# Kernel optimization log

Measured on AMD Instinct MI355X. Metric: run time of the kernel, lower is better.

Reference implementation:

```python
import jax, jax.numpy as jnp
import numpy as np

BOS_IDX = 1


def setup_inputs() -> dict:
    key = jax.random.key(0)
    ks = jax.random.split(key, 12)
    B, T, S, H, L, V = 16, 128, 64, 512, 2, 32000
    s = 0.05
    return {
        "encoder_outputs": jax.random.normal(ks[0], (B, S, H), jnp.float32),
        "encoder_h": jax.random.normal(ks[1], (L, B, H), jnp.float32) * s,
        "encoder_c": jax.random.normal(ks[2], (L, B, H), jnp.float32) * s,
        "target_tensor": jax.random.randint(ks[3], (B, T), 0, V),
        "embedding": jax.random.normal(ks[4], (V, H), jnp.float32) * s,
        "W_ih": jax.random.normal(ks[5], (L, 4 * H, H), jnp.float32) * s,
        "W_hh": jax.random.normal(ks[6], (L, 4 * H, H), jnp.float32) * s,
        "b_ih": jax.random.normal(ks[7], (L, 4 * H), jnp.float32) * s,
        "b_hh": jax.random.normal(ks[8], (L, 4 * H), jnp.float32) * s,
        "W_out": jax.random.normal(ks[9], (V, H), jnp.float32) * s,
        "b_out": jax.random.normal(ks[10], (V,), jnp.float32) * s,
    }


def reference(encoder_outputs, encoder_h, encoder_c, target_tensor,
              embedding, W_ih, W_hh, b_ih, b_hh, W_out, b_out):
    B, T = target_tensor.shape
    L = W_ih.shape[0]
    # Teacher-forced inputs: BOS then target[:, :-1]
    tokens = jnp.concatenate(
        [jnp.full((B, 1), BOS_IDX, dtype=target_tensor.dtype),
         target_tensor[:, :-1]], axis=1)  # [B, T]
    x = jax.nn.relu(embedding[tokens])  # [B, T, H]
    # The original loop resets (h, c) to encoder_states at EVERY step, so all
    # T single-step LSTM cells are independent -> vectorize over T.
    h_last, c_last = [], []
    for l in range(L):
        h0 = encoder_h[l]  # [B, H]
        c0 = encoder_c[l][:, None, :]  # [B, 1, H]
        gates = (jnp.einsum('bth,gh->btg', x, W_ih[l]) + b_ih[l]
                 + (jnp.einsum('bh,gh->bg', h0, W_hh[l]) + b_hh[l])[:, None, :])
        i, f, g, o = jnp.split(gates, 4, axis=-1)  # torch gate order i,f,g,o
        c = jax.nn.sigmoid(f) * c0 + jax.nn.sigmoid(i) * jnp.tanh(g)
        h = jax.nn.sigmoid(o) * jnp.tanh(c)  # [B, T, H]
        h_last.append(h[:, -1, :])
        c_last.append(c[:, -1, :])
        x = h  # input to next layer (dropout=0 / eval)
    logits = jnp.einsum('bth,vh->btv', x, W_out) + b_out  # [B, T, V]
    return logits, (jnp.stack(h_last), jnp.stack(c_last))
```

## Files before the change

kernel.cpp:

```cpp
#include <hip/hip_runtime.h>
#include <hip/hip_bf16.h>

typedef __bf16 bf16_t;
typedef __bf16 bf16x8 __attribute__((ext_vector_type(8)));
typedef __bf16 bf16x4 __attribute__((ext_vector_type(4)));
typedef float f32x4 __attribute__((ext_vector_type(4)));

#define B_ 16
#define T_ 128
#define H_ 512
#define L_ 2
#define V_ 32000
#define G_ 2048
#define M_ 2048

#define BN 128
#define BK 64

__device__ __forceinline__ float sigf(float x) { return 1.f / (1.f + __expf(-x)); }
__device__ __forceinline__ float tanhf_(float x) { return 2.f / (1.f + __expf(-2.f * x)) - 1.f; }


__global__ __launch_bounds__(256) void prep(const float* __restrict__ emb,
                                            const int* __restrict__ target,
                                            const float* __restrict__ enc_h,
                                            const float* __restrict__ W_ih,
                                            const float* __restrict__ W_hh,
                                            const float* __restrict__ b_ih,
                                            const float* __restrict__ b_hh,
                                            const float* __restrict__ W_out,
                                            bf16_t* __restrict__ x,
                                            bf16_t* __restrict__ wih_b,
                                            bf16_t* __restrict__ wout_b,
                                            float* __restrict__ biasall) {
    const int blk = blockIdx.x;
    const int tid = threadIdx.x;
    if (blk < 256) {
        int idx = blk * 256 + tid;
        int b = idx & 15;
        int c = (idx >> 4) & (G_ - 1);
        int l = idx >> 15;
        int gate = (c >> 4) & 3;
        int h = ((c >> 6) << 4) | (c & 15);
        int r = gate * H_ + h;
        const float* hrow = enc_h + ((size_t)l * B_ + b) * H_;
        const float* wrow = W_hh + ((size_t)l * G_ + r) * H_;
        float acc = b_ih[l * G_ + r] + b_hh[l * G_ + r];
        #pragma unroll 4
        for (int k = 0; k < H_; k += 4) {
            float4 hv = *(const float4*)(hrow + k);
            float4 wv = *(const float4*)(wrow + k);
            acc += hv.x * wv.x + hv.y * wv.y + hv.z * wv.z + hv.w * wv.w;
        }
        biasall[((size_t)l * B_ + b) * G_ + c] = acc;
    } else if (blk < 2304) {
        int idx = (blk - 256) * 256 + tid;
        int k4 = idx & 127;
        int c  = (idx >> 7) & (G_ - 1);
        int l  = idx >> 18;
        int gate = (c >> 4) & 3;
        int h = ((c >> 6) << 4) | (c & 15);
        int r = gate * H_ + h;
        float4 v = *(const float4*)(W_ih + ((size_t)l * G_ + r) * H_ + k4 * 4);
        bf16x4 o;
        o[0] = (bf16_t)v.x; o[1] = (bf16_t)v.y; o[2] = (bf16_t)v.z; o[3] = (bf16_t)v.w;
        *(bf16x4*)(wih_b + ((size_t)l * G_ + c) * H_ + k4 * 4) = o;
    } else if (blk < 3328) {
        int idx = (blk - 2304) * 256 + tid;
        int m  = idx >> 7;
        int h4 = (idx & 127) << 2;
        int b = m >> 7, t = m & 127;
        int tok = (t == 0) ? 1 : target[b * T_ + t - 1];
        float4 v = *(const float4*)(emb + (size_t)tok * H_ + h4);
        bf16x4 o;
        o[0] = (bf16_t)fmaxf(v.x, 0.f);
        o[1] = (bf16_t)fmaxf(v.y, 0.f);
        o[2] = (bf16_t)fmaxf(v.z, 0.f);
        o[3] = (bf16_t)fmaxf(v.w, 0.f);
        *(bf16x4*)(x + (size_t)m * H_ + h4) = o;
    } else {
        int idx = (blk - 3328) * 256 + tid;
        const float4* p = (const float4*)W_out + (size_t)idx * 2;
        float4 v0 = p[0], v1 = p[1];
        bf16x8 o;
        o[0] = (bf16_t)v0.x; o[1] = (bf16_t)v0.y; o[2] = (bf16_t)v0.z; o[3] = (bf16_t)v0.w;
        o[4] = (bf16_t)v1.x; o[5] = (bf16_t)v1.y; o[6] = (bf16_t)v1.z; o[7] = (bf16_t)v1.w;
        ((bf16x8*)wout_b)[idx] = o;
    }
}

template<int BMt>
__global__ __launch_bounds__(256) void gemm_gates(const bf16_t* __restrict__ A,
                                                  const bf16_t* __restrict__ B,
                                                  const float* __restrict__ bias,
                                                  int M, int N, int K,
                                                  const float* __restrict__ enc_c,
                                                  bf16_t* __restrict__ xout,
                                                  float* __restrict__ out_h,
                                                  float* __restrict__ out_c,
                                                  int l) {
    constexpr int MIc = BMt / 32;
    constexpr int NA  = BMt / 8;
    constexpr int NB  = BN / 8;
    __shared__ __align__(16) bf16_t As[BMt * BK];
    __shared__ __align__(16) bf16_t Bs[BN * BK];

    const int tid  = threadIdx.x;
    const int lane = tid & 63;
    const int wave = tid >> 6;
    const int wm = wave >> 1, wn = wave & 1;
    const int quad = lane >> 4;
    const int r16  = lane & 15;

    const int nwg = gridDim.x;
    const int q  = nwg >> 3;
    const int wg = (blockIdx.x & 7) * q + (blockIdx.x >> 3);
    const int nbx = M / BMt;
    const int bx = wg % nbx;
    const int by = wg / nbx;
    const int tileM = bx * BMt;
    const int tileN = by * BN;

    const int srow = lane >> 3;
    const int scol = (((lane & 7) ^ (lane >> 3)) << 3);

    f32x4 acc[MIc][4];
    #pragma unroll
    for (int i = 0; i < MIc; i++)
        #pragma unroll
        for (int j = 0; j < 4; j++) acc[i][j] = (f32x4){0.f, 0.f, 0.f, 0.f};

    const int nk = K / BK;
    for (int kt = 0; kt < nk; ++kt) {
        const int k0 = kt * BK;
        #pragma unroll
        for (int ii = 0; ii < (NA + NB) / 4; ++ii) {
            const int i = ii * 4 + wave;
            const bf16_t* src;
            bf16_t* dst;
            if (i < NA) {
                const int r0 = i * 8;
                src = A + (size_t)(tileM + r0 + srow) * K + k0 + scol;
                dst = As + r0 * BK;
            } else {
                const int r0 = (i - NA) * 8;
                src = B + (size_t)(tileN + r0 + srow) * K + k0 + scol;
                dst = Bs + r0 * BK;
            }
            __builtin_amdgcn_global_load_lds(
                (const __attribute__((address_space(1))) void*)src,
                (__attribute__((address_space(3))) void*)dst, 16, 0, 0);
        }
        __syncthreads();

        #pragma unroll
        for (int ks = 0; ks < 2; ++ks) {
            bf16x8 af[MIc], bfr[4];
            const int ub = ks * 4 + quad;
            #pragma unroll
            for (int mi = 0; mi < MIc; mi++) {
                const int row = wm * (BMt / 2) + mi * 16 + r16;
                af[mi] = *(const bf16x8*)(As + row * BK + ((ub ^ (r16 & 7)) << 3));
            }
            #pragma unroll
            for (int ni = 0; ni < 4; ni++) {
                const int row = wn * 64 + ni * 16 + r16;
                bfr[ni] = *(const bf16x8*)(Bs + row * BK + ((ub ^ (r16 & 7)) << 3));
            }
            #pragma unroll
            for (int mi = 0; mi < MIc; mi++)
                #pragma unroll
                for (int ni = 0; ni < 4; ni++)
                    acc[mi][ni] = __builtin_amdgcn_mfma_f32_16x16x32_bf16(
                        af[mi], bfr[ni], acc[mi][ni], 0, 0, 0);
        }
        __syncthreads();
    }

    const int b = tileM >> 7;
    const float* brow = bias + (size_t)b * G_;
    float bv[4];
    #pragma unroll
    for (int g = 0; g < 4; g++)
        bv[g] = brow[tileN + wn * 64 + g * 16 + r16];
    const int h = (2 * by + wn) * 16 + r16;
    const float c0 = enc_c[((size_t)l * B_ + b) * H_ + h];
    #pragma unroll
    for (int mi = 0; mi < MIc; mi++) {
        #pragma unroll
        for (int rr = 0; rr < 4; rr++) {
            const int t = (tileM & 127) + wm * (BMt / 2) + mi * 16 + quad * 4 + rr;
            const float gi = acc[mi][0][rr] + bv[0];
            const float gf = acc[mi][1][rr] + bv[1];
            const float gg = acc[mi][2][rr] + bv[2];
            const float go = acc[mi][3][rr] + bv[3];
            const float c = sigf(gf) * c0 + sigf(gi) * tanhf_(gg);
            const float hv = sigf(go) * tanhf_(c);
            xout[(size_t)(b * T_ + t) * H_ + h] = (bf16_t)hv;
            if (t == T_ - 1) {
                out_h[((size_t)l * B_ + b) * H_ + h] = hv;
                out_c[((size_t)l * B_ + b) * H_ + h] = c;
            }
        }
    }
}

#define LBM 128
#define LBN 256
#define LBK 64
#define LNK 8
__global__ __launch_bounds__(512, 1) void gemm_logits(const bf16_t* __restrict__ A,
                                                      const bf16_t* __restrict__ B,
                                                      float* __restrict__ C,
                                                      const float* __restrict__ bias) {
    __shared__ __align__(16) bf16_t Abuf[3][LBM * LBK];
    __shared__ __align__(16) bf16_t Bbuf[3][LBN * LBK];

    const int tid  = threadIdx.x;
    const int lane = tid & 63;
    const int wave = tid >> 6;
    const int wm = wave >> 2, wn = wave & 3;
    const int quad = lane >> 4;
    const int r16  = lane & 15;

    const int wg = (blockIdx.x & 7) * 250 + (blockIdx.x >> 3);
    const int tileM = (wg & 15) * LBM;
    const int tileN = (wg >> 4) * LBN;

    const int srow = lane >> 3;
    const int scol = (((lane & 7) ^ srow) << 3);

    f32x4 acc[4][4];
    #pragma unroll
    for (int i = 0; i < 4; i++)
        #pragma unroll
        for (int j = 0; j < 4; j++) acc[i][j] = (f32x4){0.f, 0.f, 0.f, 0.f};

    auto issue = [&](int t, int buf) {
        const int k0 = t * LBK;
        #pragma unroll
        for (int i = 0; i < 6; ++i) {
            const int rbase = (i < 2 ? i * 64 : (i - 2) * 64) + wave * 8;
            if (i < 2) {
                const bf16_t* src = A + (size_t)(tileM + rbase + srow) * H_ + k0 + scol;
                __builtin_amdgcn_global_load_lds(
                    (const __attribute__((address_space(1))) void*)src,
                    (__attribute__((address_space(3))) void*)(&Abuf[buf][rbase * LBK]),
                    16, 0, 0);
            } else {
                const bf16_t* src = B + (size_t)(tileN + rbase + srow) * H_ + k0 + scol;
                __builtin_amdgcn_global_load_lds(
                    (const __attribute__((address_space(1))) void*)src,
                    (__attribute__((address_space(3))) void*)(&Bbuf[buf][rbase * LBK]),
                    16, 0, 0);
            }
        }
    };

    issue(0, 0);
    issue(1, 1);
    asm volatile("s_waitcnt vmcnt(6)" ::: "memory");
    __builtin_amdgcn_sched_barrier(0);
    __builtin_amdgcn_s_barrier();
    __builtin_amdgcn_sched_barrier(0);

    #pragma unroll
    for (int j = 0; j < LNK; ++j) {
        const int jb = j % 3;
        if (j + 2 < LNK) issue(j + 2, (j + 2) % 3);
        __builtin_amdgcn_sched_barrier(0);

        bf16x8 af[4][2], bfv[4][2];
        #pragma unroll
        for (int ks = 0; ks < 2; ++ks) {
            const int ub = ks * 4 + quad;
            const int pu = (ub ^ (r16 & 7)) << 3;
            #pragma unroll
            for (int mi = 0; mi < 4; mi++)
                af[mi][ks] = *(const bf16x8*)(&Abuf[jb][(wm * 64 + mi * 16 + r16) * LBK + pu]);
            #pragma unroll
            for (int ni = 0; ni < 4; ni++)
                bfv[ni][ks] = *(const bf16x8*)(&Bbuf[jb][(wn * 64 + ni * 16 + r16) * LBK + pu]);
        }

        __builtin_amdgcn_s_setprio(1);
        #pragma unroll
        for (int ks = 0; ks < 2; ++ks)
            #pragma unroll
            for (int mi = 0; mi < 4; mi++)
                #pragma unroll
                for (int ni = 0; ni < 4; ni++)
                    acc[mi][ni] = __builtin_amdgcn_mfma_f32_16x16x32_bf16(
                        af[mi][ks], bfv[ni][ks], acc[mi][ni], 0, 0, 0);
        __builtin_amdgcn_s_setprio(0);

        if (j < LNK - 1) {
            if (j < LNK - 2) { asm volatile("s_waitcnt vmcnt(6)" ::: "memory"); }
            else             { asm volatile("s_waitcnt vmcnt(0)" ::: "memory"); }
            __builtin_amdgcn_sched_barrier(0);
            __builtin_amdgcn_s_barrier();
            __builtin_amdgcn_sched_barrier(0);
        }
    }

    #pragma unroll
    for (int mi = 0; mi < 4; mi++) {
        #pragma unroll
        for (int ni = 0; ni < 4; ni++) {
            const int col = tileN + wn * 64 + ni * 16 + r16;
            const float bv = bias[col];
            #pragma unroll
            for (int rr = 0; rr < 4; rr++) {
                const int row = tileM + wm * 64 + mi * 16 + quad * 4 + rr;
                __builtin_nontemporal_store(acc[mi][ni][rr] + bv,
                                            &C[(size_t)row * V_ + col]);
            }
        }
    }
}

extern "C" void kernel_launch(void* const* d_in, const int* in_sizes, int n_in,
                              void* d_out, int out_size, void* d_ws, size_t ws_size,
                              hipStream_t stream) {
    const float* enc_h  = (const float*)d_in[1];
    const float* enc_c  = (const float*)d_in[2];
    const int*   target = (const int*)d_in[3];
    const float* emb    = (const float*)d_in[4];
    const float* W_ih   = (const float*)d_in[5];
    const float* W_hh   = (const float*)d_in[6];
    const float* b_ih   = (const float*)d_in[7];
    const float* b_hh   = (const float*)d_in[8];
    const float* W_out  = (const float*)d_in[9];
    const float* b_out  = (const float*)d_in[10];
    float* out = (float*)d_out;

    char* w = (char*)d_ws;
    bf16_t* x       = (bf16_t*)(w);
    bf16_t* wih_b   = (bf16_t*)(w + 2097152);
    bf16_t* wout_b  = (bf16_t*)(w + 6291456);
    bf16_t* x2      = (bf16_t*)(w + 39059456);
    float*  biasall = (float*)(w + 55836672);

    float* out_h = out + (size_t)M_ * V_;
    float* out_c = out_h + (size_t)L_ * B_ * H_;

    prep<<<11328, 256, 0, stream>>>(emb, target, enc_h, W_ih, W_hh, b_ih, b_hh,
                                    W_out, x, wih_b, wout_b, biasall);

    gemm_gates<64><<<(M_ / 64) * (G_ / BN), 256, 0, stream>>>(
        x, wih_b, biasall, M_, G_, H_,
        enc_c, x2, out_h, out_c, 0);
    gemm_gates<64><<<(M_ / 64) * (G_ / BN), 256, 0, stream>>>(
        x2, wih_b + (size_t)G_ * H_, biasall + (size_t)B_ * G_,
        M_, G_, H_, enc_c, x, out_h, out_c, 1);

    gemm_logits<<<(M_ / LBM) * (V_ / LBN), 512, 0, stream>>>(x, wout_b, out, b_out);
}
```

Before: 468.5 us.

## Fuse W_out conversion into gates kernels and simplify logits GEMM to 256 threads

Moves the W_out fp32-to-bf16 conversion out of the prep kernel and splits it across the two gates kernels as extra blocks, so the memory-bound conversion can overlap with the small gate GEMMs. The gates GEMM is de-templated with hardcoded sizes. The logits GEMM drops its triple-buffered 512-thread pipeline with explicit waitcnt for a simple single-buffer 256-thread kernel with 128x256 tiles per block and more accumulators per wave. This risks losing load/compute overlap and raising register pressure in the dominant logits GEMM.

After: 504.6 us. 1.08x slower.

```diff
diff --git a/kernel.cpp b/kernel.cpp
--- a/kernel.cpp
+++ b/kernel.cpp
@@ -14,9 +14,6 @@
 #define G_ 2048
 #define M_ 2048
 
-#define BN 128
-#define BK 64
-
 __device__ __forceinline__ float sigf(float x) { return 1.f / (1.f + __expf(-x)); }
 __device__ __forceinline__ float tanhf_(float x) { return 2.f / (1.f + __expf(-2.f * x)) - 1.f; }
 
@@ -28,10 +25,8 @@
                                             const float* __restrict__ W_hh,
                                             const float* __restrict__ b_ih,
                                             const float* __restrict__ b_hh,
-                                            const float* __restrict__ W_out,
                                             bf16_t* __restrict__ x,
                                             bf16_t* __restrict__ wih_b,
-                                            bf16_t* __restrict__ wout_b,
                                             float* __restrict__ biasall) {
     const int blk = blockIdx.x;
     const int tid = threadIdx.x;
@@ -65,7 +60,7 @@
         bf16x4 o;
         o[0] = (bf16_t)v.x; o[1] = (bf16_t)v.y; o[2] = (bf16_t)v.z; o[3] = (bf16_t)v.w;
         *(bf16x4*)(wih_b + ((size_t)l * G_ + c) * H_ + k4 * 4) = o;
-    } else if (blk < 3328) {
+    } else {
         int idx = (blk - 2304) * 256 + tid;
         int m  = idx >> 7;
         int h4 = (idx & 127) << 2;
@@ -78,32 +73,32 @@
         o[2] = (bf16_t)fmaxf(v.z, 0.f);
         o[3] = (bf16_t)fmaxf(v.w, 0.f);
         *(bf16x4*)(x + (size_t)m * H_ + h4) = o;
-    } else {
-        int idx = (blk - 3328) * 256 + tid;
+    }
+}
+
+__global__ __launch_bounds__(256) void gates_cvt(const bf16_t* __restrict__ A,
+                                                 const bf16_t* __restrict__ B,
+                                                 const float* __restrict__ bias,
+                                                 const float* __restrict__ enc_c,
+                                                 bf16_t* __restrict__ xout,
+                                                 float* __restrict__ out_h,
+                                                 float* __restrict__ out_c,
+                                                 int l,
+                                                 const float* __restrict__ W_out,
+                                                 bf16_t* __restrict__ wout_b) {
+    if (blockIdx.x >= 512) {
+        int idx = (blockIdx.x - 512) * 256 + threadIdx.x + l * 1024000;
         const float4* p = (const float4*)W_out + (size_t)idx * 2;
         float4 v0 = p[0], v1 = p[1];
         bf16x8 o;
         o[0] = (bf16_t)v0.x; o[1] = (bf16_t)v0.y; o[2] = (bf16_t)v0.z; o[3] = (bf16_t)v0.w;
         o[4] = (bf16_t)v1.x; o[5] = (bf16_t)v1.y; o[6] = (bf16_t)v1.z; o[7] = (bf16_t)v1.w;
         ((bf16x8*)wout_b)[idx] = o;
-    }
-}
-
-template<int BMt>
-__global__ __launch_bounds__(256) void gemm_gates(const bf16_t* __restrict__ A,
-                                                  const bf16_t* __restrict__ B,
-                                                  const float* __restrict__ bias,
-                                                  int M, int N, int K,
-                                                  const float* __restrict__ enc_c,
-                                                  bf16_t* __restrict__ xout,
-                                                  float* __restrict__ out_h,
-                                                  float* __restrict__ out_c,
-                                                  int l) {
-    constexpr int MIc = BMt / 32;
-    constexpr int NA  = BMt / 8;
-    constexpr int NB  = BN / 8;
-    __shared__ __align__(16) bf16_t As[BMt * BK];
-    __shared__ __align__(16) bf16_t Bs[BN * BK];
+        return;
+    }
+    constexpr int BM = 64, GBN = 128, BK = 64;
+    __shared__ __align__(16) bf16_t As[BM * BK];
+    __shared__ __align__(16) bf16_t Bs[GBN * BK];
 
     const int tid  = threadIdx.x;
     const int lane = tid & 63;
@@ -112,40 +107,35 @@
     const int quad = lane >> 4;
     const int r16  = lane & 15;
 
-    const int nwg = gridDim.x;
-    const int q  = nwg >> 3;
-    const int wg = (blockIdx.x & 7) * q + (blockIdx.x >> 3);
-    const int nbx = M / BMt;
-    const int bx = wg % nbx;
-    const int by = wg / nbx;
-    const int tileM = bx * BMt;
-    const int tileN = by * BN;
+    const int wg = (blockIdx.x & 7) * 64 + (blockIdx.x >> 3);
+    const int bx = wg & 31;
+    const int by = wg >> 5;
+    const int tileM = bx * BM;
+    const int tileN = by * GBN;
 
     const int srow = lane >> 3;
-    const int scol = (((lane & 7) ^ (lane >> 3)) << 3);
-
-    f32x4 acc[MIc][4];
-    #pragma unroll
-    for (int i = 0; i < MIc; i++)
+    const int scol = (((lane & 7) ^ srow) << 3);
+
+    f32x4 acc[2][4];
+    #pragma unroll
+    for (int i = 0; i < 2; i++)
         #pragma unroll
         for (int j = 0; j < 4; j++) acc[i][j] = (f32x4){0.f, 0.f, 0.f, 0.f};
 
-    const int nk = K / BK;
-    for (int kt = 0; kt < nk; ++kt) {
+    for (int kt = 0; kt < H_ / BK; ++kt) {
         const int k0 = kt * BK;
         #pragma unroll
-        for (int ii = 0; ii < (NA + NB) / 4; ++ii) {
+        for (int ii = 0; ii < 6; ++ii) {
             const int i = ii * 4 + wave;
             const bf16_t* src;
             bf16_t* dst;
-            if (i < NA) {
-                const int r0 = i * 8;
-                src = A + (size_t)(tileM + r0 + srow) * K + k0 + scol;
-                dst = As + r0 * BK;
+            if (i < 8) {
+                src = A + (size_t)(tileM + i * 8 + srow) * H_ + k0 + scol;
+                dst = As + i * 8 * BK;
             } else {
-                const int r0 = (i - NA) * 8;
-                src = B + (size_t)(tileN + r0 + srow) * K + k0 + scol;
-                dst = Bs + r0 * BK;
+                const int j = i - 8;
+                src = B + (size_t)(tileN + j * 8 + srow) * H_ + k0 + scol;
+                dst = Bs + j * 8 * BK;
             }
             __builtin_amdgcn_global_load_lds(
                 (const __attribute__((address_space(1))) void*)src,
@@ -155,20 +145,17 @@
 
         #pragma unroll
         for (int ks = 0; ks < 2; ++ks) {
-            bf16x8 af[MIc], bfr[4];
+            bf16x8 af[2], bfr[4];
             const int ub = ks * 4 + quad;
-            #pragma unroll
-            for (int mi = 0; mi < MIc; mi++) {
-                const int row = wm * (BMt / 2) + mi * 16 + r16;
-                af[mi] = *(const bf16x8*)(As + row * BK + ((ub ^ (r16 & 7)) << 3));
-            }
-            #pragma unroll
-            for (int ni = 0; ni < 4; ni++) {
-                const int row = wn * 64 + ni * 16 + r16;
-                bfr[ni] = *(const bf16x8*)(Bs + row * BK + ((ub ^ (r16 & 7)) << 3));
-            }
-            #pragma unroll
-            for (int mi = 0; mi < MIc; mi++)
+            const int pu = (ub ^ (r16 & 7)) << 3;
+            #pragma unroll
+            for (int mi = 0; mi < 2; mi++)
+                af[mi] = *(const bf16x8*)(As + (wm * 32 + mi * 16 + r16) * BK + pu);
+            #pragma unroll
+            for (int ni = 0; ni < 4; ni++)
+                bfr[ni] = *(const bf16x8*)(Bs + (wn * 64 + ni * 16 + r16) * BK + pu);
+            #pragma unroll
+            for (int mi = 0; mi < 2; mi++)
                 #pragma unroll
                 for (int ni = 0; ni < 4; ni++)
                     acc[mi][ni] = __builtin_amdgcn_mfma_f32_16x16x32_bf16(
@@ -186,10 +173,10 @@
     const int h = (2 * by + wn) * 16 + r16;
     const float c0 = enc_c[((size_t)l * B_ + b) * H_ + h];
     #pragma unroll
-    for (int mi = 0; mi < MIc; mi++) {
+    for (int mi = 0; mi < 2; mi++) {
         #pragma unroll
         for (int rr = 0; rr < 4; rr++) {
-            const int t = (tileM & 127) + wm * (BMt / 2) + mi * 16 + quad * 4 + rr;
+            const int t = (tileM & 127) + wm * 32 + mi * 16 + quad * 4 + rr;
             const float gi = acc[mi][0][rr] + bv[0];
             const float gf = acc[mi][1][rr] + bv[1];
             const float gg = acc[mi][2][rr] + bv[2];
@@ -208,18 +195,17 @@
 #define LBM 128
 #define LBN 256
 #define LBK 64
-#define LNK 8
-__global__ __launch_bounds__(512, 1) void gemm_logits(const bf16_t* __restrict__ A,
-                                                      const bf16_t* __restrict__ B,
-                                                      float* __restrict__ C,
-                                                      const float* __restrict__ bias) {
-    __shared__ __align__(16) bf16_t Abuf[3][LBM * LBK];
-    __shared__ __align__(16) bf16_t Bbuf[3][LBN * LBK];
+__global__ __launch_bounds__(256) void gemm_logits(const bf16_t* __restrict__ A,
+                                                   const bf16_t* __restrict__ B,
+                                                   float* __restrict__ C,
+                                                   const float* __restrict__ bias) {
+    __shared__ __align__(16) bf16_t As[LBM * LBK];
+    __shared__ __align__(16) bf16_t Bs[LBN * LBK];
 
     const int tid  = threadIdx.x;
     const int lane = tid & 63;
     const int wave = tid >> 6;
-    const int wm = wave >> 2, wn = wave & 3;
+    const int wm = wave >> 1, wn = wave & 1;
     const int quad = lane >> 4;
     const int r16  = lane & 15;
 
@@ -230,84 +216,61 @@
     const int srow = lane >> 3;
     const int scol = (((lane & 7) ^ srow) << 3);
 
-    f32x4 acc[4][4];
+    f32x4 acc[4][8];
     #pragma unroll
     for (int i = 0; i < 4; i++)
         #pragma unroll
-        for (int j = 0; j < 4; j++) acc[i][j] = (f32x4){0.f, 0.f, 0.f, 0.f};
-
-    auto issue = [&](int t, int buf) {
-        const int k0 = t * LBK;
-        #pragma unroll
-        for (int i = 0; i < 6; ++i) {
-            const int rbase = (i < 2 ? i * 64 : (i - 2) * 64) + wave * 8;
-            if (i < 2) {
-                const bf16_t* src = A + (size_t)(tileM + rbase + srow) * H_ + k0 + scol;
-                __builtin_amdgcn_global_load_lds(
-                    (const __attribute__((address_space(1))) void*)src,
-                    (__attribute__((address_space(3))) void*)(&Abuf[buf][rbase * LBK]),
-                    16, 0, 0);
+        for (int j = 0; j < 8; j++) acc[i][j] = (f32x4){0.f, 0.f, 0.f, 0.f};
+
+    for (int kt = 0; kt < H_ / LBK; ++kt) {
+        const int k0 = kt * LBK;
+        #pragma unroll
+        for (int ii = 0; ii < 12; ++ii) {
+            const int i = ii * 4 + wave;
+            const bf16_t* src;
+            bf16_t* dst;
+            if (i < 16) {
+                src = A + (size_t)(tileM + i * 8 + srow) * H_ + k0 + scol;
+                dst = As + i * 8 * LBK;
             } else {
-                const bf16_t* src = B + (size_t)(tileN + rbase + srow) * H_ + k0 + scol;
-                __builtin_amdgcn_global_load_lds(
-                    (const __attribute__((address_space(1))) void*)src,
-                    (__attribute__((address_space(3))) void*)(&Bbuf[buf][rbase * LBK]),
-                    16, 0, 0);
+                const int j = i - 16;
+                src = B + (size_t)(tileN + j * 8 + srow) * H_ + k0 + scol;
+                dst = Bs + j * 8 * LBK;
             }
-        }
-    };
-
-    issue(0, 0);
-    issue(1, 1);
-    asm volatile("s_waitcnt vmcnt(6)" ::: "memory");
-    __builtin_amdgcn_sched_barrier(0);
-    __builtin_amdgcn_s_barrier();
-    __builtin_amdgcn_sched_barrier(0);
-
-    #pragma unroll
-    for (int j = 0; j < LNK; ++j) {
-        const int jb = j % 3;
-        if (j + 2 < LNK) issue(j + 2, (j + 2) % 3);
-        __builtin_amdgcn_sched_barrier(0);
-
-        bf16x8 af[4][2], bfv[4][2];
+            __builtin_amdgcn_global_load_lds(
+                (const __attribute__((address_space(1))) void*)src,
+                (__attribute__((address_space(3))) void*)dst, 16, 0, 0);
+        }
+        __syncthreads();
+
         #pragma unroll
         for (int ks = 0; ks < 2; ++ks) {
+            bf16x8 af[4], bfr[8];
             const int ub = ks * 4 + quad;
             const int pu = (ub ^ (r16 & 7)) << 3;
             #pragma unroll
             for (int mi = 0; mi < 4; mi++)
-                af[mi][ks] = *(const bf16x8*)(&Abuf[jb][(wm * 64 + mi * 16 + r16) * LBK + pu]);
-            #pragma unroll
-            for (int ni = 0; ni < 4; ni++)
-                bfv[ni][ks] = *(const bf16x8*)(&Bbuf[jb][(wn * 64 + ni * 16 + r16) * LBK + pu]);
-        }
-
-        __builtin_amdgcn_s_setprio(1);
-        #pragma unroll
-        for (int ks = 0; ks < 2; ++ks)
+                af[mi] = *(const bf16x8*)(As + (wm * 64 + mi * 16 + r16) * LBK + pu);
+            #pragma unroll
+            for (int ni = 0; ni < 8; ni++)
+                bfr[ni] = *(const bf16x8*)(Bs + (wn * 128 + ni * 16 + r16) * LBK + pu);
+            __builtin_amdgcn_s_setprio(1);
             #pragma unroll
             for (int mi = 0; mi < 4; mi++)
                 #pragma unroll
-                for (int ni = 0; ni < 4; ni++)
+                for (int ni = 0; ni < 8; ni++)
                     acc[mi][ni] = __builtin_amdgcn_mfma_f32_16x16x32_bf16(
-                        af[mi][ks], bfv[ni][ks], acc[mi][ni], 0, 0, 0);
-        __builtin_amdgcn_s_setprio(0);
-
-        if (j < LNK - 1) {
-            if (j < LNK - 2) { asm volatile("s_waitcnt vmcnt(6)" ::: "memory"); }
-            else             { asm volatile("s_waitcnt vmcnt(0)" ::: "memory"); }
-            __builtin_amdgcn_sched_barrier(0);
-            __builtin_amdgcn_s_barrier();
-            __builtin_amdgcn_sched_barrier(0);
-        }
+                        af[mi], bfr[ni], acc[mi][ni], 0, 0, 0);
+            __builtin_amdgcn_s_setprio(0);
+        }
+        __syncthreads();
     }
 
     #pragma unroll
     for (int mi = 0; mi < 4; mi++) {
         #pragma unroll
-        for (int ni = 0; ni < 4; ni++) {
-            const int col = tileN + wn * 64 + ni * 16 + r16;
+        for (int ni = 0; ni < 8; ni++) {
+            const int col = tileN + wn * 128 + ni * 16 + r16;
             const float bv = bias[col];
             #pragma unroll
             for (int rr = 0; rr < 4; rr++) {
@@ -344,15 +307,14 @@
     float* out_h = out + (size_t)M_ * V_;
     float* out_c = out_h + (size_t)L_ * B_ * H_;
 
-    prep<<<11328, 256, 0, stream>>>(emb, target, enc_h, W_ih, W_hh, b_ih, b_hh,
-                                    W_out, x, wih_b, wout_b, biasall);
-
-    gemm_gates<64><<<(M_ / 64) * (G_ / BN), 256, 0, stream>>>(
-        x, wih_b, biasall, M_, G_, H_,
-        enc_c, x2, out_h, out_c, 0);
-    gemm_gates<64><<<(M_ / 64) * (G_ / BN), 256, 0, stream>>>(
+    prep<<<3328, 256, 0, stream>>>(emb, target, enc_h, W_ih, W_hh, b_ih, b_hh,
+                                   x, wih_b, biasall);
+
+    gates_cvt<<<4512, 256, 0, stream>>>(
+        x, wih_b, biasall, enc_c, x2, out_h, out_c, 0, W_out, wout_b);
+    gates_cvt<<<4512, 256, 0, stream>>>(
         x2, wih_b + (size_t)G_ * H_, biasall + (size_t)B_ * G_,
-        M_, G_, H_, enc_c, x, out_h, out_c, 1);
-
-    gemm_logits<<<(M_ / LBM) * (V_ / LBN), 512, 0, stream>>>(x, wout_b, out, b_out);
+        enc_c, x, out_h, out_c, 1, W_out, wout_b);
+
+    gemm_logits<<<(M_ / LBM) * (V_ / LBN), 256, 0, stream>>>(x, wout_b, out, b_out);
 }
```
